# Kernel tuning notes

Hardware: AMD Instinct MI355X
Metric: run time of the kernel (lower is better)

## Reference

```python
import jax, jax.numpy as jnp
import numpy as np
from jax import lax

EPSILON = 1e-12


def _sobel_kernels(n1=1, n2=2, n3=2):
    Sx = np.asarray([[[-n1, 0, n1], [-n2, 0, n2], [-n1, 0, n1]],
                     [[-n2, 0, n2], [-n3 * n2, 0, n3 * n2], [-n2, 0, n2]],
                     [[-n1, 0, n1], [-n2, 0, n2], [-n1, 0, n1]]])
    Sy = np.asarray([[[-n1, -n2, -n1], [0, 0, 0], [n1, n2, n1]],
                     [[-n2, -n3 * n2, -n2], [0, 0, 0], [n2, n3 * n2, n2]],
                     [[-n1, -n2, -n1], [0, 0, 0], [n1, n2, n1]]])
    Sz = np.asarray([[[-n1, -n2, -n1], [-n2, -n3 * n2, -n2], [-n1, -n2, -n1]],
                     [[0, 0, 0], [0, 0, 0], [0, 0, 0]],
                     [[n1, n2, n1], [n2, n3 * n2, n2], [n1, n2, n1]]])
    Sd11 = np.asarray([[[0, n1, n2], [-n1, 0, n1], [-n2, -n1, 0]],
                       [[0, n2, n2 * n3], [-n2, 0, n2], [-n2 * n3, -n2, 0]],
                       [[0, n1, n2], [-n1, 0, n1], [-n2, -n1, 0]]])
    Sd12 = np.asarray([[[-n2, -n1, 0], [-n1, 0, n1], [0, n1, n2]],
                       [[-n2 * n3, -n2, 0], [-n2, 0, n2], [0, n2, n2 * n3]],
                       [[-n2, -n1, 0], [-n1, 0, n1], [0, n1, n2]]])
    Sd21 = Sd11.T
    Sd22 = Sd12.T
    Sd31 = np.asarray([-S.T for S in Sd11.T])
    Sd32 = np.asarray([S.T for S in Sd12.T])
    ks = np.stack([Sx, Sy, Sz, Sd11, Sd12, Sd21, Sd22, Sd31, Sd32]).astype(np.float32)
    return jnp.asarray(ks[:, None])  # [9, 1, 3, 3, 3] (OIDHW)


_KERNELS = _sobel_kernels(1, 2, 2)


def _edge_magnitude(img):
    # img: [B, C, H, W, D]. Per-channel convs are summed over C in the original;
    # by linearity of conv, sum channels first, then run all 9 stencils at once.
    C = img.shape[1]
    x = jnp.sum(img, axis=1, keepdims=True)  # [B, 1, H, W, D]
    g = lax.conv_general_dilated(
        x, _KERNELS, window_strides=(1, 1, 1), padding='SAME',
        dimension_numbers=('NCDHW', 'OIDHW', 'NCDHW'))  # [B, 9, H, W, D]
    mag = jnp.sqrt(jnp.sum(g * g, axis=1, keepdims=True) + EPSILON)
    return mag / C  # (1/C) * sqrt(sum_sq + eps), matches operator precedence


def setup_inputs() -> dict:
    key = jax.random.key(0)
    k1, k2 = jax.random.split(key)
    shape = (2, 2, 128, 128, 128)
    y = jax.random.normal(k1, shape, dtype=jnp.float32)
    yp = jax.random.normal(k2, shape, dtype=jnp.float32)
    return {"y": y, "yp": yp}


def reference(y, yp):
    y_edge = _edge_magnitude(y)
    yp_edge = _edge_magnitude(yp)
    return jnp.mean((y_edge - yp_edge) ** 2)  # nn.MSELoss default 'mean'
```

## Files before the change

### kernel.cpp

```cpp
#include <hip/hip_runtime.h>


namespace {

typedef float v2f __attribute__((ext_vector_type(2)));

constexpr int ZDIM = 128, YDIM = 128, XDIM = 128;
constexpr int TX = 64, TY = 4, ZC = 16;
constexpr int XW  = XDIM / 2;
constexpr int YX2 = YDIM * XW;
constexpr size_t CS2 = (size_t)ZDIM * YX2;
constexpr float INV_N = 1.0f / 4194304.0f;

__device__ __forceinline__ float bperm(int addr, float v) {
  return __int_as_float(__builtin_amdgcn_ds_bpermute(addr, __float_as_int(v)));
}

__device__ __forceinline__ v2f vfma(v2f a, v2f b, v2f c) {
  return __builtin_elementwise_fma(a, b, c);
}

__device__ __forceinline__ v2f vsplat(float x) { v2f r = {x, x}; return r; }

__device__ __forceinline__ v2f emag_ss(const v2f* __restrict__ Ca,
                                       const v2f* __restrict__ Cb,
                                       const v2f* __restrict__ Cc) {
  const v2f two = vsplat(2.0f);
  const v2f g1  = vfma(two, Cb[0], Ca[0] + Cc[0]);
  const v2f g2  = vfma(two, Cb[1], Ca[1] + Cc[1]);
  const v2f g3  = Cc[2] - Ca[2];
  const v2f Azx = vfma(two, Cb[3], Ca[3] + Cc[3]);
  const v2f Azy = vfma(two, Cb[4], Ca[4] + Cc[4]);
  const v2f Axz = Cc[5] - Ca[5];
  const v2f Axy = g2 - Cb[1];
  const v2f Ayx = g1 - Cb[0];
  const v2f Ayz = Cc[6] - Ca[6];
  const v2f g4 = Azx - Azy, g5 = Azx + Azy;
  const v2f g6 = Axz - Axy, g7 = Axz + Axy;
  const v2f g8 = Ayx - Ayz, g9 = Ayx + Ayz;
  v2f s = vfma(g1, g1, vsplat(1e-12f));
  s = vfma(g2, g2, s); s = vfma(g3, g3, s);
  s = vfma(g4, g4, s); s = vfma(g5, g5, s);
  s = vfma(g6, g6, s); s = vfma(g7, g7, s);
  s = vfma(g8, g8, s); s = vfma(g9, g9, s);
  return s;
}

__global__ __launch_bounds__(256)
void gme_loss_kernel(const float* __restrict__ y,
                     const float* __restrict__ yp,
                     float* __restrict__ out) {
  const int lane = threadIdx.x;
  const int ty   = threadIdx.y;
  const int tid  = ty * TX + lane;

  const int yy = blockIdx.x * TY + ty;
  const int z0 = blockIdx.y * ZC;
  const int b  = blockIdx.z;

  const v2f* Y0 = (const v2f*)y  + (size_t)b * 2 * CS2;
  const v2f* Y1 = Y0 + CS2;
  const v2f* P0 = (const v2f*)yp + (size_t)b * 2 * CS2;
  const v2f* P1 = P0 + CS2;

  const int yM = yy > 0 ? yy - 1 : 0;
  const int yP = yy < YDIM - 1 ? yy + 1 : YDIM - 1;
  const int oM = yM * XW + lane;
  const int oC = yy * XW + lane;
  const int oP = yP * XW + lane;
  const float mm = (yy > 0) ? 1.0f : 0.0f;
  const float mp = (yy < YDIM - 1) ? 1.0f : 0.0f;

  const int addrL = (lane > 0 ? lane - 1 : 0) << 2;
  const int addrR = (lane < TX - 1 ? lane + 1 : TX - 1) << 2;
  const float lz = (lane == 0) ? 0.0f : 1.0f;
  const float rz = (lane == TX - 1) ? 0.0f : 1.0f;

  v2f pf[3][12];
  v2f KY[2][7], KP[2][7];
  v2f accv = {0.0f, 0.0f};

  auto loadRaw = [&](int buf, int zc) {
    const int zca = zc < 0 ? 0 : (zc > ZDIM - 1 ? ZDIM - 1 : zc);
    const int o   = zca * YX2;
    pf[buf][0]  = Y0[o + oM]; pf[buf][1]  = Y1[o + oM];
    pf[buf][2]  = P0[o + oM]; pf[buf][3]  = P1[o + oM];
    pf[buf][4]  = Y0[o + oC]; pf[buf][5]  = Y1[o + oC];
    pf[buf][6]  = P0[o + oC]; pf[buf][7]  = P1[o + oC];
    pf[buf][8]  = Y0[o + oP]; pf[buf][9]  = Y1[o + oP];
    pf[buf][10] = P0[o + oP]; pf[buf][11] = P1[o + oP];
  };

  auto combos = [&](v2f ys, v2f yd, v2f ye, v2f* __restrict__ C) {
    const float ysl = bperm(addrL, ys.y) * lz, ysr = bperm(addrR, ys.x) * rz;
    const float ydl = bperm(addrL, yd.y) * lz, ydr = bperm(addrR, yd.x) * rz;
    const float yel = bperm(addrL, ye.y) * lz, yer = bperm(addrR, ye.x) * rz;
    const v2f ysL = {ysl, ys.x}, ysR = {ys.y, ysr};
    const v2f ydL = {ydl, yd.x}, ydR = {yd.y, ydr};
    const v2f yeL = {yel, ye.x}, yeR = {ye.y, yer};
    const v2f tS = ysL + ysR, tD = ydL + ydR, tE = yeL + yeR;
    C[0] = ysR - ysL;
    C[2] = vfma(vsplat(2.0f), ys, tS);
    C[6] = tS + ys;
    C[1] = vfma(vsplat(2.0f), yd, tD);
    C[4] = tD + yd;
    C[3] = yeR - yeL;
    C[5] = vfma(vsplat(2.0f), ye, tE);
  };

  loadRaw(0, z0 - 1);
  loadRaw(1, z0);

#pragma unroll 6
  for (int j = 0; j < ZC + 2; ++j) {
    loadRaw((j + 2) % 3, z0 + 1 + j);

    const int   zc = z0 - 1 + j;
    const float fz = ((unsigned)zc < (unsigned)ZDIM) ? 1.0f : 0.0f;
    const v2f* q = pf[j % 3];
    const v2f smY = (q[0] + q[1])  * vsplat(fz * mm);
    const v2f smP = (q[2] + q[3])  * vsplat(fz * mm);
    const v2f scY = (q[4] + q[5])  * vsplat(fz);
    const v2f scP = (q[6] + q[7])  * vsplat(fz);
    const v2f spY = (q[8] + q[9])  * vsplat(fz * mp);
    const v2f spP = (q[10] + q[11]) * vsplat(fz * mp);

    v2f Cy[7], Cp[7];
    {
      const v2f tt = smY + spY;
      combos(vfma(vsplat(2.0f), scY, tt), spY - smY, tt + scY, Cy);
    }
    {
      const v2f tt = smP + spP;
      combos(vfma(vsplat(2.0f), scP, tt), spP - smP, tt + scP, Cp);
    }

    if (j >= 2) {
      const v2f ssY = emag_ss(KY[j % 2], KY[(j + 1) % 2], Cy);
      const v2f ssP = emag_ss(KP[j % 2], KP[(j + 1) % 2], Cp);
      v2f d;
      d.x = 0.5f * (__builtin_amdgcn_sqrtf(ssY.x) - __builtin_amdgcn_sqrtf(ssP.x));
      d.y = 0.5f * (__builtin_amdgcn_sqrtf(ssY.y) - __builtin_amdgcn_sqrtf(ssP.y));
      accv = vfma(d, d, accv);
    }

#pragma unroll
    for (int k = 0; k < 7; ++k) { KY[j % 2][k] = Cy[k]; KP[j % 2][k] = Cp[k]; }
  }

  __shared__ float red[4];
  float acc = accv.x + accv.y;
#pragma unroll
  for (int off = 32; off > 0; off >>= 1) acc += __shfl_down(acc, off);
  if (lane == 0) red[ty] = acc;
  __syncthreads();
  if (tid == 0) {
    const float s = (red[0] + red[1] + red[2] + red[3]) * INV_N;
    atomicAdd(out, s);
  }
}

}

extern "C" void kernel_launch(void* const* d_in, const int* in_sizes, int n_in,
                              void* d_out, int out_size, void* d_ws, size_t ws_size,
                              hipStream_t stream) {
  const float* y  = (const float*)d_in[0];
  const float* yp = (const float*)d_in[1];
  float* out = (float*)d_out;

  hipMemsetAsync(out, 0, sizeof(float), stream);

  dim3 block(TX, TY, 1);
  dim3 grid(YDIM / TY,
            ZDIM / ZC,
            2);
  gme_loss_kernel<<<grid, block, 0, stream>>>(y, yp, out);
}
```

Baseline: 107.2 us.

## Keep raw y-row sums per plane and compute full 3D stencil per output

Instead of carrying seven x/y-combined intermediates per plane and combining them across z, the kernel now keeps only the six channel-summed row values per z-plane in a three-deep ring. For each output it recomputes the z, then y, then x separable combinations. The prefetch buffer shrinks from triple to double, the z chunk is halved, the loop is fully unrolled, and launch bounds request higher occupancy. This cuts register pressure and raises parallelism, at the cost of more cross-lane permutes (14 per volume instead of 6 per plane) and more halo reloads.

Result: slower. 168.1 us (+56.8%).

```diff
diff --git a/kernel.cpp b/kernel.cpp
--- a/kernel.cpp
+++ b/kernel.cpp
@@ -6,7 +6,7 @@
 typedef float v2f __attribute__((ext_vector_type(2)));
 
 constexpr int ZDIM = 128, YDIM = 128, XDIM = 128;
-constexpr int TX = 64, TY = 4, ZC = 16;
+constexpr int TX = 64, TY = 4, ZC = 8;
 constexpr int XW  = XDIM / 2;
 constexpr int YX2 = YDIM * XW;
 constexpr size_t CS2 = (size_t)ZDIM * YX2;
@@ -22,31 +22,7 @@
 
 __device__ __forceinline__ v2f vsplat(float x) { v2f r = {x, x}; return r; }
 
-__device__ __forceinline__ v2f emag_ss(const v2f* __restrict__ Ca,
-                                       const v2f* __restrict__ Cb,
-                                       const v2f* __restrict__ Cc) {
-  const v2f two = vsplat(2.0f);
-  const v2f g1  = vfma(two, Cb[0], Ca[0] + Cc[0]);
-  const v2f g2  = vfma(two, Cb[1], Ca[1] + Cc[1]);
-  const v2f g3  = Cc[2] - Ca[2];
-  const v2f Azx = vfma(two, Cb[3], Ca[3] + Cc[3]);
-  const v2f Azy = vfma(two, Cb[4], Ca[4] + Cc[4]);
-  const v2f Axz = Cc[5] - Ca[5];
-  const v2f Axy = g2 - Cb[1];
-  const v2f Ayx = g1 - Cb[0];
-  const v2f Ayz = Cc[6] - Ca[6];
-  const v2f g4 = Azx - Azy, g5 = Azx + Azy;
-  const v2f g6 = Axz - Axy, g7 = Axz + Axy;
-  const v2f g8 = Ayx - Ayz, g9 = Ayx + Ayz;
-  v2f s = vfma(g1, g1, vsplat(1e-12f));
-  s = vfma(g2, g2, s); s = vfma(g3, g3, s);
-  s = vfma(g4, g4, s); s = vfma(g5, g5, s);
-  s = vfma(g6, g6, s); s = vfma(g7, g7, s);
-  s = vfma(g8, g8, s); s = vfma(g9, g9, s);
-  return s;
-}
-
-__global__ __launch_bounds__(256)
+__global__ __launch_bounds__(256, 4)
 void gme_loss_kernel(const float* __restrict__ y,
                      const float* __restrict__ yp,
                      float* __restrict__ out) {
@@ -76,8 +52,8 @@
   const float lz = (lane == 0) ? 0.0f : 1.0f;
   const float rz = (lane == TX - 1) ? 0.0f : 1.0f;
 
-  v2f pf[3][12];
-  v2f KY[2][7], KP[2][7];
+  v2f pf[2][12];
+  v2f R[3][6];
   v2f accv = {0.0f, 0.0f};
 
   auto loadRaw = [&](int buf, int zc) {
@@ -91,61 +67,95 @@
     pf[buf][10] = P0[o + oP]; pf[buf][11] = P1[o + oP];
   };
 
-  auto combos = [&](v2f ys, v2f yd, v2f ye, v2f* __restrict__ C) {
-    const float ysl = bperm(addrL, ys.y) * lz, ysr = bperm(addrR, ys.x) * rz;
-    const float ydl = bperm(addrL, yd.y) * lz, ydr = bperm(addrR, yd.x) * rz;
-    const float yel = bperm(addrL, ye.y) * lz, yer = bperm(addrR, ye.x) * rz;
-    const v2f ysL = {ysl, ys.x}, ysR = {ys.y, ysr};
-    const v2f ydL = {ydl, yd.x}, ydR = {yd.y, ydr};
-    const v2f yeL = {yel, ye.x}, yeR = {ye.y, yer};
-    const v2f tS = ysL + ysR, tD = ydL + ydR, tE = yeL + yeR;
-    C[0] = ysR - ysL;
-    C[2] = vfma(vsplat(2.0f), ys, tS);
-    C[6] = tS + ys;
-    C[1] = vfma(vsplat(2.0f), yd, tD);
-    C[4] = tD + yd;
-    C[3] = yeR - yeL;
-    C[5] = vfma(vsplat(2.0f), ye, tE);
+  auto sumPlane = [&](int rs, int buf, float fz) {
+    const v2f* q = pf[buf];
+    R[rs][0] = (q[0] + q[1])   * vsplat(fz * mm);
+    R[rs][3] = (q[2] + q[3])   * vsplat(fz * mm);
+    R[rs][1] = (q[4] + q[5])   * vsplat(fz);
+    R[rs][4] = (q[6] + q[7])   * vsplat(fz);
+    R[rs][2] = (q[8] + q[9])   * vsplat(fz * mp);
+    R[rs][5] = (q[10] + q[11]) * vsplat(fz * mp);
+  };
+
+  auto volSS = [&](const v2f* za, const v2f* zb, const v2f* zc2) -> v2f {
+    const v2f two = vsplat(2.0f);
+    v2f zs[3], zd[3], ze[3];
+#pragma unroll
+    for (int r = 0; r < 3; ++r) {
+      const v2f t = za[r] + zc2[r];
+      zs[r] = vfma(two, zb[r], t);
+      zd[r] = zc2[r] - za[r];
+      ze[r] = t + zb[r];
+    }
+    const v2f t1 = zs[0] + zs[2];
+    const v2f ss = vfma(two, zs[1], t1);
+    const v2f sd = zs[2] - zs[0];
+    const v2f se = t1 + zs[1];
+    const v2f t2 = zd[0] + zd[2];
+    const v2f ds = vfma(two, zd[1], t2);
+    const v2f de = t2 + zd[1];
+    const v2f t3 = ze[0] + ze[2];
+    const v2f es = vfma(two, ze[1], t3);
+    const v2f ed = ze[2] - ze[0];
+
+    auto DX = [&](v2f q) -> v2f {
+      const float l  = bperm(addrL, q.y) * lz;
+      const float r2 = bperm(addrR, q.x) * rz;
+      v2f o; o.x = q.y - l; o.y = r2 - q.x; return o;
+    };
+    auto SX = [&](v2f q) -> v2f {
+      const float l  = bperm(addrL, q.y) * lz;
+      const float r2 = bperm(addrR, q.x) * rz;
+      v2f t; t.x = l + q.y; t.y = q.x + r2;
+      return vfma(two, q, t);
+    };
+    auto SXEX = [&](v2f q, v2f& ex) -> v2f {
+      const float l  = bperm(addrL, q.y) * lz;
+      const float r2 = bperm(addrR, q.x) * rz;
+      v2f t; t.x = l + q.y; t.y = q.x + r2;
+      ex = t + q;
+      return vfma(two, q, t);
+    };
+
+    const v2f g1 = DX(ss);
+    v2f ex_sd;  const v2f g2 = SXEX(sd, ex_sd);
+    v2f ex_ds;  const v2f g3 = SXEX(ds, ex_ds);
+    const v2f dxse = DX(se);
+    const v2f sxde = SX(de);
+    const v2f sxed = SX(ed);
+    const v2f dxes = DX(es);
+    const v2f g4 = dxse - ex_sd, g5 = dxse + ex_sd;
+    const v2f g6 = sxde - sxed, g7 = sxde + sxed;
+    const v2f g8 = dxes - ex_ds, g9 = dxes + ex_ds;
+
+    v2f s = vfma(g1, g1, vsplat(1e-12f));
+    s = vfma(g2, g2, s); s = vfma(g3, g3, s);
+    s = vfma(g4, g4, s); s = vfma(g5, g5, s);
+    s = vfma(g6, g6, s); s = vfma(g7, g7, s);
+    s = vfma(g8, g8, s); s = vfma(g9, g9, s);
+    return s;
   };
 
   loadRaw(0, z0 - 1);
   loadRaw(1, z0);
 
-#pragma unroll 6
+#pragma unroll
   for (int j = 0; j < ZC + 2; ++j) {
-    loadRaw((j + 2) % 3, z0 + 1 + j);
-
     const int   zc = z0 - 1 + j;
     const float fz = ((unsigned)zc < (unsigned)ZDIM) ? 1.0f : 0.0f;
-    const v2f* q = pf[j % 3];
-    const v2f smY = (q[0] + q[1])  * vsplat(fz * mm);
-    const v2f smP = (q[2] + q[3])  * vsplat(fz * mm);
-    const v2f scY = (q[4] + q[5])  * vsplat(fz);
-    const v2f scP = (q[6] + q[7])  * vsplat(fz);
-    const v2f spY = (q[8] + q[9])  * vsplat(fz * mp);
-    const v2f spP = (q[10] + q[11]) * vsplat(fz * mp);
-
-    v2f Cy[7], Cp[7];
-    {
-      const v2f tt = smY + spY;
-      combos(vfma(vsplat(2.0f), scY, tt), spY - smY, tt + scY, Cy);
-    }
-    {
-      const v2f tt = smP + spP;
-      combos(vfma(vsplat(2.0f), scP, tt), spP - smP, tt + scP, Cp);
-    }
-
+    sumPlane(j % 3, j % 2, fz);
+    loadRaw(j % 2, z0 + 1 + j);
     if (j >= 2) {
-      const v2f ssY = emag_ss(KY[j % 2], KY[(j + 1) % 2], Cy);
-      const v2f ssP = emag_ss(KP[j % 2], KP[(j + 1) % 2], Cp);
+      const v2f* Ra = R[(j - 2) % 3];
+      const v2f* Rb = R[(j - 1) % 3];
+      const v2f* Rc = R[j % 3];
+      const v2f ssY = volSS(Ra + 0, Rb + 0, Rc + 0);
+      const v2f ssP = volSS(Ra + 3, Rb + 3, Rc + 3);
       v2f d;
       d.x = 0.5f * (__builtin_amdgcn_sqrtf(ssY.x) - __builtin_amdgcn_sqrtf(ssP.x));
       d.y = 0.5f * (__builtin_amdgcn_sqrtf(ssY.y) - __builtin_amdgcn_sqrtf(ssP.y));
       accv = vfma(d, d, accv);
     }
-
-#pragma unroll
-    for (int k = 0; k < 7; ++k) { KY[j % 2][k] = Cy[k]; KP[j % 2][k] = Cp[k]; }
   }
 
   __shared__ float red[4];
```
